# Kernel optimization log

Measured on AMD Instinct MI355X. Metric: run time of the kernel, lower is better.

## Reference

```python
import jax, jax.numpy as jnp
import numpy as np
from jax import lax

K = 5  # up_kernel_size

def nearest_up2(x):
    # PyTorch F.interpolate(scale_factor=2) default mode='nearest': out[i]=in[i//2]
    return jnp.repeat(jnp.repeat(x, 2, axis=2), 2, axis=3)

def conv1x1(x, W, b=None):
    # x: [B,C,H,W], W: [O,C]
    y = jnp.einsum('bchw,oc->bohw', x, W)
    if b is not None:
        y = y + b[None, :, None, None]
    return y

def depthwise3x3(x, W, b):
    # x: [B,25,H,W], W: [25,1,3,3] (OIHW with groups=25)
    y = lax.conv_general_dilated(x, W, window_strides=(1, 1), padding='SAME',
                                 feature_group_count=x.shape[1],
                                 dimension_numbers=('NCHW', 'OIHW', 'NCHW'))
    return y + b[None, :, None, None]

def carafe(de, kernels):
    # de: [B,C,H,W]; kernels: [B,K*K,2H,2W], softmax-normalized over channel dim
    B, C, H, Wd = de.shape
    r = K // 2
    de_p = jnp.pad(de, ((0, 0), (0, 0), (r, r), (r, r)))
    # patches[b,k,c,h,w] = de neighborhood, k = dy*K+dx  -> [B,25,C,H,W]
    patches = jnp.stack([de_p[:, :, dy:dy + H, dx:dx + Wd]
                         for dy in range(K) for dx in range(K)], axis=1)
    # kernels[b,k,2h+s,2w+t] -> [B,25,H,2,W,2]; source pixel is (i//2, j//2)
    kr = kernels.reshape(B, K * K, H, 2, Wd, 2)
    out = jnp.einsum('bkchw,bkhswt->bchswt', patches, kr)
    return out.reshape(B, C, 2 * H, 2 * Wd)

def setup_inputs() -> dict:
    key = jax.random.key(0)
    ks = jax.random.split(key, 8)
    B, C, H, W = 4, 256, 64, 64
    en = jax.random.normal(ks[0], (B, C, 2 * H, 2 * W), dtype=jnp.float32)
    de = jax.random.normal(ks[1], (B, C, H, W), dtype=jnp.float32)
    s = 1.0 / np.sqrt(C)
    W_gate = jax.random.uniform(ks[2], (1, C), jnp.float32, -s, s)
    b_gate = jnp.zeros((1,), jnp.float32)
    W_ce = jax.random.uniform(ks[3], (K * K, C), jnp.float32, -s, s)
    b_ce = jnp.zeros((K * K,), jnp.float32)
    W_cd = jax.random.uniform(ks[4], (K * K, C), jnp.float32, -s, s)
    W_dw = jax.random.uniform(ks[5], (K * K, 1, 3, 3), jnp.float32, -0.33, 0.33)
    b_dw = jnp.zeros((K * K,), jnp.float32)
    return {'en': en, 'de': de, 'W_gate': W_gate, 'b_gate': b_gate,
            'W_ce': W_ce, 'b_ce': b_ce, 'W_cd': W_cd, 'W_dw': W_dw, 'b_dw': b_dw}

def reference(en, de, W_gate, b_gate, W_ce, b_ce, W_cd, W_dw, b_dw):
    # gate generator
    gate = jax.nn.sigmoid(nearest_up2(conv1x1(de, W_gate, b_gate)))  # [B,1,2H,2W]
    # kernel generator (SemiShiftDepthWise)
    enc = conv1x1(en, W_ce, b_ce)      # [B,25,2H,2W]
    dec = conv1x1(de, W_cd)            # [B,25,H,W]
    raw = depthwise3x3(enc, W_dw, b_dw) + nearest_up2(depthwise3x3(dec, W_dw, b_dw))
    kernels = jax.nn.softmax(raw, axis=1)
    return gate * en + (1.0 - gate) * carafe(de, kernels)
```

## Files before the change

kernel.cpp:

```cpp
#include <hip/hip_runtime.h>


typedef unsigned short u16;
typedef unsigned int u32;
typedef float v2f __attribute__((ext_vector_type(2)));

#define NB 4
#define NC 256
#define NH 64
#define NW 64
#define NH2 128
#define NW2 128

#define OFF_WG   0
#define OFF_BG   256
#define OFF_WCE  272
#define OFF_BCE  6672
#define OFF_WCD  6704
#define OFF_WDW  13104
#define OFF_BDW  13330
#define OFF_FLAG 13356

#define OFF_GATE 16384
#define OFF_KB   32768
#define OFF_ENC  851968
#define OFF_DEC  2490368
#define OFF_DET  851968
#define OFF_P1   851968
#define FULL_NEED_BYTES 12877824ull

#define NGATE 16384
#define NDEC  20480
#define NENC  122880
#define NKBF  532480

__device__ __forceinline__ float bf2f(u16 u){ return __uint_as_float(((u32)u) << 16); }
__device__ __forceinline__ u16 f2bf(float f){
  u32 x = __float_as_uint(f);
  return (u16)((x + 0x7fffu + ((x >> 16) & 1u)) >> 16);
}
__device__ __forceinline__ float ldin(const void* p, int i, bool f32){
  return f32 ? ((const float*)p)[i] : bf2f(((const u16*)p)[i]);
}

__global__ __launch_bounds__(256) void k_detect(const void* de_raw, float* ws){
  __shared__ int cnt;
  if (threadIdx.x == 0) cnt = 0;
  __syncthreads();
  int c = 0;
#pragma unroll
  for (int s = 0; s < 2; s++) {
    int i = (threadIdx.x + s * 256) * 2;
    u16 u = ((const u16*)de_raw)[i];
    int e = (u >> 7) & 0xff;
    if (e >= 0x70 && e <= 0x82) c++;
  }
  atomicAdd(&cnt, c);
  __syncthreads();
  if (threadIdx.x == 0) ws[OFF_FLAG] = (cnt < 256) ? 1.0f : 0.0f;
}

__global__ __launch_bounds__(256) void k_prep(const void* Wg, const void* bg,
    const void* Wce, const void* bce, const void* Wcd, const void* Wdw, const void* bdw,
    float* ws){
  bool f = ws[OFF_FLAG] != 0.f;
  int i = threadIdx.x + blockIdx.x * 256;
  if (i < 6400) {
    ws[OFF_WCE + i] = ldin(Wce, i, f);
    ws[OFF_WCD + i] = ldin(Wcd, i, f);
    if (i < 256) ws[OFF_WG + i] = ldin(Wg, i, f);
    if (i < 1)   ws[OFF_BG + i] = ldin(bg, i, f);
    if (i < 25)  ws[OFF_BCE + i] = ldin(bce, i, f);
    if (i < 225) ws[OFF_WDW + i] = ldin(Wdw, i, f);
    if (i < 25)  ws[OFF_BDW + i] = ldin(bdw, i, f);
  }
}


__global__ __launch_bounds__(256) void o1a_dec_gate(const void* de, float* ws){
  __shared__ float red[4][26][64];
  bool f = ws[OFF_FLAG] != 0.f;
  int b = blockIdx.x >> 7;
  int rem = blockIdx.x & 127;
  int h = rem >> 1;
  int chunk = rem & 1;
  int g = threadIdx.x >> 6;
  int w = threadIdx.x & 63;
  int c0 = __builtin_amdgcn_readfirstlane(chunk * 128 + g * 32);
  float acc[26];
#pragma unroll
  for (int o = 0; o < 26; o++) acc[o] = 0.f;
  int idx = ((b * NC + c0) * NH + h) * NW + w;
  for (int ci = 0; ci < 32; ci += 8) {
    float v0 = ldin(de, idx,            f);
    float v1 = ldin(de, idx + 1 * 4096, f);
    float v2 = ldin(de, idx + 2 * 4096, f);
    float v3 = ldin(de, idx + 3 * 4096, f);
    float v4 = ldin(de, idx + 4 * 4096, f);
    float v5 = ldin(de, idx + 5 * 4096, f);
    float v6 = ldin(de, idx + 6 * 4096, f);
    float v7 = ldin(de, idx + 7 * 4096, f);
    idx += 8 * 4096;
    int c = c0 + ci;
    acc[25] += ws[OFF_WG + c] * v0 + ws[OFF_WG + c + 1] * v1
             + ws[OFF_WG + c + 2] * v2 + ws[OFF_WG + c + 3] * v3
             + ws[OFF_WG + c + 4] * v4 + ws[OFF_WG + c + 5] * v5
             + ws[OFF_WG + c + 6] * v6 + ws[OFF_WG + c + 7] * v7;
#pragma unroll
    for (int k = 0; k < 25; k++) {
      const float* wk = ws + OFF_WCD + k * 256 + c;
      acc[k] += wk[0] * v0 + wk[1] * v1 + wk[2] * v2 + wk[3] * v3
              + wk[4] * v4 + wk[5] * v5 + wk[6] * v6 + wk[7] * v7;
    }
  }
#pragma unroll
  for (int o = 0; o < 26; o++) red[g][o][w] = acc[o];
  __syncthreads();
  for (int item = threadIdx.x; item < 26 * 64; item += 256) {
    int o = item >> 6; int ww = item & 63;
    float s = red[0][o][ww] + red[1][o][ww] + red[2][o][ww] + red[3][o][ww];
    ws[OFF_P1 + (((chunk * NB + b) * 26 + o) << 12) + (h << 6) + ww] = s;
  }
}

__global__ __launch_bounds__(256) void o1b_reduce(float* ws){
  int i = blockIdx.x * 256 + threadIdx.x;
  int b = i / (26 * 4096);
  int r = i - b * 26 * 4096;
  int o = r >> 12;
  int pix = r & 4095;
  float s = ws[OFF_P1 + (((0 * NB + b) * 26 + o) << 12) + pix]
          + ws[OFF_P1 + (((1 * NB + b) * 26 + o) << 12) + pix];
  if (o < 25)
    ws[OFF_DEC + ((b * 25 + o) << 12) + pix] = s;
  else {
    float z = s + ws[OFF_BG];
    ws[OFF_GATE + (b << 12) + pix] = 1.f / (1.f + __expf(-z));
  }
}

__global__ __launch_bounds__(256) void o2_det(const void* de, float* ws){
  __shared__ float tile[64][65];
  bool f = ws[OFF_FLAG] != 0.f;
  u16* det = (u16*)(ws + OFF_DET);
  int b = blockIdx.x / 272;
  int r = blockIdx.x % 272;
  int p = r >> 2;
  int c0 = (r & 3) << 6;
  int h = p - 2;
  bool hv = (h >= 0 && h < NH);
  for (int item = threadIdx.x; item < 64 * 64; item += 256) {
    int cl = item >> 6, w = item & 63;
    float v = hv ? ldin(de, ((b * NC + c0 + cl) * NH + h) * NW + w, f) : 0.f;
    tile[w][cl] = v;
  }
  __syncthreads();
  u16* dst = det + ((b * 68 + p) * 68) * NC + c0;
  for (int item = threadIdx.x; item < 68 * 64; item += 256) {
    int q = item >> 6, cl = item & 63;
    int w = q - 2;
    float v = (w >= 0 && w < NW) ? tile[w][cl] : 0.f;
    dst[q * NC + cl] = f2bf(v);
  }
}

__global__ __launch_bounds__(256) void o3_enc(const void* en, float* ws){
  __shared__ float red[4][25][64];
  bool f = ws[OFF_FLAG] != 0.f;
  int b = blockIdx.x >> 8;
  int rem = blockIdx.x & 255;
  int y = rem >> 1;
  int xs = (rem & 1) << 6;
  int g = threadIdx.x >> 6;
  int xl = threadIdx.x & 63;
  int c0 = __builtin_amdgcn_readfirstlane(g * 64);
  float acc[25];
#pragma unroll
  for (int k = 0; k < 25; k++) acc[k] = 0.f;
  int idx = ((b * NC + c0) * NH2 + y) * NW2 + xs + xl;
  for (int ci = 0; ci < 64; ci += 8) {
    float v0 = ldin(en, idx,             f);
    float v1 = ldin(en, idx + 1 * 16384, f);
    float v2 = ldin(en, idx + 2 * 16384, f);
    float v3 = ldin(en, idx + 3 * 16384, f);
    float v4 = ldin(en, idx + 4 * 16384, f);
    float v5 = ldin(en, idx + 5 * 16384, f);
    float v6 = ldin(en, idx + 6 * 16384, f);
    float v7 = ldin(en, idx + 7 * 16384, f);
    idx += 8 * 16384;
    int c = c0 + ci;
#pragma unroll
    for (int k = 0; k < 25; k++) {
      const float* wk = ws + OFF_WCE + k * 256 + c;
      acc[k] += wk[0] * v0 + wk[1] * v1 + wk[2] * v2 + wk[3] * v3
              + wk[4] * v4 + wk[5] * v5 + wk[6] * v6 + wk[7] * v7;
    }
  }
#pragma unroll
  for (int k = 0; k < 25; k++) red[g][k][xl] = acc[k];
  __syncthreads();
  for (int item = threadIdx.x; item < 25 * 64; item += 256) {
    int k = item >> 6; int xx = item & 63;
    float s = red[0][k][xx] + red[1][k][xx] + red[2][k][xx] + red[3][k][xx]
            + ws[OFF_BCE + k];
    ws[OFF_ENC + ((b * 25 + k) * NH2 + y) * NW2 + xs + xx] = s;
  }
}

__global__ __launch_bounds__(256) void o4_kernels(float* ws){
  __shared__ float red[25][64];
  int b = blockIdx.x >> 8;
  int rem = blockIdx.x & 255;
  int y = rem >> 1;
  int xs = (rem & 1) << 6;
  int tg = __builtin_amdgcn_readfirstlane(threadIdx.x >> 6);
  int xl = threadIdx.x & 63;
  int x = xs + xl;
  int h = y >> 1, w = x >> 1;
  const float* enc = ws + OFF_ENC + (b * 25) * NH2 * NW2;
  const float* dec = ws + OFF_DEC + (b * 25) * NH * NW;

  for (int k = tg; k < 25; k += 4) {
    float s = 2.f * ws[OFF_BDW + k];
#pragma unroll
    for (int u = 0; u < 3; u++) {
      int yy = y + u - 1, hh = h + u - 1;
      bool yok = (yy >= 0 && yy < NH2);
      bool hok = (hh >= 0 && hh < NH);
#pragma unroll
      for (int v = 0; v < 3; v++) {
        int xx = x + v - 1, w2 = w + v - 1;
        float wd = ws[OFF_WDW + k * 9 + u * 3 + v];
        if (yok && xx >= 0 && xx < NW2)
          s += enc[(k * NH2 + yy) * NW2 + xx] * wd;
        if (hok && w2 >= 0 && w2 < NW)
          s += dec[(k * NH + hh) * NW + w2] * wd;
      }
    }
    red[k][xl] = s;
  }
  __syncthreads();

  if (threadIdx.x < 64) {
    int t = threadIdx.x;
    int xp = xs + t;
    float m = -1e30f;
#pragma unroll
    for (int k = 0; k < 25; k++) m = fmaxf(m, red[k][t]);
    float sum = 0.f;
#pragma unroll
    for (int k = 0; k < 25; k++) {
      float e = __expf(red[k][t] - m);
      red[k][t] = e;
      sum += e;
    }
    float inv = 1.f / sum;
    int st = ((y & 1) << 1) + (xp & 1);
    int wp = xp >> 1;
    u16* kbu = (u16*)(ws + OFF_KB);
    u16* dst = kbu + ((b * NH + h) * NW + wp) * 100 + st;
#pragma unroll
    for (int k = 0; k < 25; k++) dst[k * 4] = f2bf(red[k][t] * inv);
  }
}

__global__ __launch_bounds__(256) void o5_final(const void* en, float* ws, float* out){
  __shared__ u16 stag[32][260];
  bool f = ws[OFF_FLAG] != 0.f;
  const u16* det = (const u16*)(ws + OFF_DET);
  const u16* kbu = (const u16*)(ws + OFF_KB);
  const float* gate = ws + OFF_GATE;

  int bi = blockIdx.x;
  int xcd = bi & 7;
  int slot = bi >> 3;
  int s = slot & 1;
  int pid = ((slot >> 1) << 3) | xcd;
  int b = pid >> 8;
  int rem = pid & 255;
  int h = rem >> 2;
  int w0b = (rem & 3) * 16;
  int wave = threadIdx.x >> 6;
  int lane = threadIdx.x & 63;
  int c4 = lane * 4;

  int wu0 = __builtin_amdgcn_readfirstlane(w0b + wave * 4);
  const u16* kp0 = kbu + ((b * NH + h) * NW + wu0) * 100 + s * 2;

  v2f acc[4][2][2];
#pragma unroll
  for (int i = 0; i < 4; i++)
#pragma unroll
    for (int t = 0; t < 2; t++)
#pragma unroll
      for (int p = 0; p < 2; p++) { acc[i][t][p].x = 0.f; acc[i][t][p].y = 0.f; }

#pragma unroll
  for (int dy = 0; dy < 5; dy++) {
    const u16* dp = det + (((b * 68 + h + dy) * 68 + wu0) * NC) + c4;
    u32 wlo[8], whi[8];
#pragma unroll
    for (int j = 0; j < 8; j++) {
      uint2 dv = *(const uint2*)(dp + j * NC);
      wlo[j] = dv.x; whi[j] = dv.y;
    }
#pragma unroll
    for (int i = 0; i < 4; i++) {
#pragma unroll
      for (int dx = 0; dx < 5; dx++) {
        int j = i + dx;
        u32 kk = *(const u32*)(kp0 + i * 100 + (dy * 5 + dx) * 4);
        v2f kp2, vA, vB;
        kp2.x = __uint_as_float(kk << 16);
        kp2.y = __uint_as_float(kk & 0xffff0000u);
        vA.x = __uint_as_float(wlo[j] << 16);
        vA.y = __uint_as_float(wlo[j] & 0xffff0000u);
        vB.x = __uint_as_float(whi[j] << 16);
        vB.y = __uint_as_float(whi[j] & 0xffff0000u);
        asm("v_pk_fma_f32 %0, %1, %2, %0 op_sel:[0,0,0] op_sel_hi:[0,1,1]"
            : "+v"(acc[i][0][0]) : "v"(kp2), "v"(vA));
        asm("v_pk_fma_f32 %0, %1, %2, %0 op_sel:[0,0,0] op_sel_hi:[0,1,1]"
            : "+v"(acc[i][0][1]) : "v"(kp2), "v"(vB));
        asm("v_pk_fma_f32 %0, %1, %2, %0 op_sel:[1,0,0] op_sel_hi:[1,1,1]"
            : "+v"(acc[i][1][0]) : "v"(kp2), "v"(vA));
        asm("v_pk_fma_f32 %0, %1, %2, %0 op_sel:[1,0,0] op_sel_hi:[1,1,1]"
            : "+v"(acc[i][1][1]) : "v"(kp2), "v"(vB));
      }
    }
  }

#pragma unroll
  for (int i = 0; i < 4; i++) {
    int xl = (wave * 4 + i) * 2;
#pragma unroll
    for (int t = 0; t < 2; t++) {
      ushort4 pv;
      pv.x = f2bf(acc[i][t][0].x); pv.y = f2bf(acc[i][t][0].y);
      pv.z = f2bf(acc[i][t][1].x); pv.w = f2bf(acc[i][t][1].y);
      *(ushort4*)&stag[xl + t][c4] = pv;
    }
  }
  __syncthreads();

  int xp = threadIdx.x & 31;
  int cb = (threadIdx.x >> 5) * 2;
  int x = w0b * 2 + xp;
  int wpix = w0b + (xp >> 1);
  int y = 2 * h + s;
  float g = gate[(b * NH + h) * NW + wpix];
  float gi = 1.f - g;
#pragma unroll
  for (int pass = 0; pass < 16; pass++) {
    int c = cb + pass * 16;
    u32 rr = *(const u32*)&stag[xp][c];
    float cr0 = bf2f((u16)(rr & 0xffffu));
    float cr1 = bf2f((u16)(rr >> 16));
    int eidx = ((b * NC + c) * NH2 + y) * NW2 + x;
    float e0 = ldin(en, eidx, f);
    float e1 = ldin(en, eidx + NH2 * NW2, f);
    __builtin_nontemporal_store(g * e0 + gi * cr0, &out[eidx]);
    __builtin_nontemporal_store(g * e1 + gi * cr1, &out[eidx + NH2 * NW2]);
  }
}


__global__ __launch_bounds__(256) void kA_gate(const void* de, float* ws, int b){
  bool f = ws[OFF_FLAG] != 0.f;
  int idx = blockIdx.x * 256 + threadIdx.x;
  int h = idx >> 6, w = idx & 63;
  float s = ws[OFF_BG];
  for (int c = 0; c < NC; c++)
    s += ldin(de, ((b * NC + c) * NH + h) * NW + w, f) * ws[OFF_WG + c];
  ws[NGATE + idx] = 1.f / (1.f + __expf(-s));
}

__global__ __launch_bounds__(256) void kB_dec(const void* de, float* ws, int b){
  bool f = ws[OFF_FLAG] != 0.f;
  int idx = blockIdx.x * 256 + threadIdx.x;
  int h = idx >> 6, w = idx & 63;
  float acc[25];
#pragma unroll
  for (int k = 0; k < 25; k++) acc[k] = 0.f;
  for (int c = 0; c < NC; c++) {
    float v = ldin(de, ((b * NC + c) * NH + h) * NW + w, f);
#pragma unroll
    for (int k = 0; k < 25; k++) acc[k] += v * ws[OFF_WCD + k * 256 + c];
  }
#pragma unroll
  for (int k = 0; k < 25; k++)
    ws[NDEC + (k * NH + h) * NW + w] = acc[k];
}

__global__ __launch_bounds__(256) void kC_enc(const void* en, float* ws, int b){
  bool f = ws[OFF_FLAG] != 0.f;
  int idx = blockIdx.x * 256 + threadIdx.x;
  int y = idx >> 7, x = idx & 127;
  float acc[25];
#pragma unroll
  for (int k = 0; k < 25; k++) acc[k] = 0.f;
  for (int c = 0; c < NC; c++) {
    float v = ldin(en, ((b * NC + c) * NH2 + y) * NW2 + x, f);
#pragma unroll
    for (int k = 0; k < 25; k++) acc[k] += v * ws[OFF_WCE + k * 256 + c];
  }
#pragma unroll
  for (int k = 0; k < 25; k++)
    ws[NENC + (k * NH2 + y) * NW2 + x] = acc[k] + ws[OFF_BCE + k];
}

__global__ __launch_bounds__(256) void kD_kern(float* ws){
  int idx = blockIdx.x * 256 + threadIdx.x;
  int y = idx >> 7, x = idx & 127;
  int h = y >> 1, w = x >> 1;
  float raw[25];
#pragma unroll
  for (int k = 0; k < 25; k++) {
    float s = 2.f * ws[OFF_BDW + k];
#pragma unroll
    for (int u = 0; u < 3; u++) {
      int yy = y + u - 1, hh = h + u - 1;
#pragma unroll
      for (int v = 0; v < 3; v++) {
        int xx = x + v - 1, ww = w + v - 1;
        float wd = ws[OFF_WDW + k * 9 + u * 3 + v];
        if (yy >= 0 && yy < NH2 && xx >= 0 && xx < NW2)
          s += ws[NENC + (k * NH2 + yy) * NW2 + xx] * wd;
        if (hh >= 0 && hh < NH && ww >= 0 && ww < NW)
          s += ws[NDEC + (k * NH + hh) * NW + ww] * wd;
      }
    }
    raw[k] = s;
  }
  float m = raw[0];
#pragma unroll
  for (int k = 1; k < 25; k++) m = fmaxf(m, raw[k]);
  float sum = 0.f;
#pragma unroll
  for (int k = 0; k < 25; k++) { raw[k] = __expf(raw[k] - m); sum += raw[k]; }
  float inv = 1.f / sum;
  float* dst = ws + NKBF + idx * 25;
#pragma unroll
  for (int k = 0; k < 25; k++) dst[k] = raw[k] * inv;
}

__global__ __launch_bounds__(256) void kE_out(const void* en, const void* de,
    const float* ws, float* out, int b){
  bool f = ws[OFF_FLAG] != 0.f;
  int idx = blockIdx.x * 256 + threadIdx.x;
  int c = idx >> 14;
  int y = (idx >> 7) & 127;
  int x = idx & 127;
  int h = y >> 1, w = x >> 1;
  const float* kb = ws + NKBF + (y * NW2 + x) * 25;
  float acc = 0.f;
#pragma unroll
  for (int dy = 0; dy < 5; dy++) {
    int hh = h + dy - 2;
    if (hh < 0 || hh >= NH) continue;
#pragma unroll
    for (int dx = 0; dx < 5; dx++) {
      int ww = w + dx - 2;
      if (ww < 0 || ww >= NW) continue;
      acc += ldin(de, ((b * NC + c) * NH + hh) * NW + ww, f) * kb[dy * 5 + dx];
    }
  }
  float g = ws[NGATE + h * NW + w];
  float e = ldin(en, ((b * NC + c) * NH2 + y) * NW2 + x, f);
  out[((b * NC + c) * NH2 + y) * NW2 + x] = g * e + (1.f - g) * acc;
}

static const void* find_by_size(void* const* d_in, const int* in_sizes, int n_in,
                                int want, int skip, const void* fb){
  int seen = 0;
  for (int i = 0; i < n_in; i++)
    if (in_sizes[i] == want) {
      if (seen == skip) return d_in[i];
      seen++;
    }
  return fb;
}

extern "C" void kernel_launch(void* const* d_in, const int* in_sizes, int n_in,
                              void* d_out, int out_size, void* d_ws, size_t ws_size,
                              hipStream_t stream) {
  (void)out_size;
  const void* en  = find_by_size(d_in, in_sizes, n_in, 4*256*128*128, 0, d_in[0]);
  const void* de  = find_by_size(d_in, in_sizes, n_in, 4*256*64*64,   0, d_in[1]);
  const void* Wg  = find_by_size(d_in, in_sizes, n_in, 256,           0, d_in[2]);
  const void* bg  = find_by_size(d_in, in_sizes, n_in, 1,             0, d_in[3]);
  const void* Wce = find_by_size(d_in, in_sizes, n_in, 6400,          0, d_in[4]);
  const void* bce = find_by_size(d_in, in_sizes, n_in, 25,            0, d_in[5]);
  const void* Wcd = find_by_size(d_in, in_sizes, n_in, 6400,          1, d_in[6]);
  const void* Wdw = find_by_size(d_in, in_sizes, n_in, 225,           0, d_in[7]);
  const void* bdw = find_by_size(d_in, in_sizes, n_in, 25,            1, d_in[8]);
  float* ws = (float*)d_ws;
  float* out = (float*)d_out;

  hipLaunchKernelGGL(k_detect, dim3(1), dim3(256), 0, stream, de, ws);
  hipLaunchKernelGGL(k_prep, dim3(25), dim3(256), 0, stream,
                     Wg, bg, Wce, bce, Wcd, Wdw, bdw, ws);

  if (ws_size >= FULL_NEED_BYTES) {
    hipLaunchKernelGGL(o1a_dec_gate, dim3(NB * NH * 2),     dim3(256), 0, stream, de, ws);
    hipLaunchKernelGGL(o1b_reduce,   dim3(1664),            dim3(256), 0, stream, ws);
    hipLaunchKernelGGL(o3_enc,       dim3(NB * NH2 * 2),    dim3(256), 0, stream, en, ws);
    hipLaunchKernelGGL(o4_kernels,   dim3(NB * NH2 * 2),    dim3(256), 0, stream, ws);
    hipLaunchKernelGGL(o2_det,       dim3(NB * 68 * 4),     dim3(256), 0, stream, de, ws);
    hipLaunchKernelGGL(o5_final,     dim3(NB * NH * 4 * 2), dim3(256), 0, stream, en, ws, out);
  } else {
    for (int b = 0; b < NB; b++) {
      hipLaunchKernelGGL(kA_gate, dim3(16),    dim3(256), 0, stream, de, ws, b);
      hipLaunchKernelGGL(kB_dec,  dim3(16),    dim3(256), 0, stream, de, ws, b);
      hipLaunchKernelGGL(kC_enc,  dim3(64),    dim3(256), 0, stream, en, ws, b);
      hipLaunchKernelGGL(kD_kern, dim3(64),    dim3(256), 0, stream, ws);
      hipLaunchKernelGGL(kE_out,  dim3(16384), dim3(256), 0, stream, en, de, ws, out, b);
    }
  }
}
```

Measured before the change: 239.9 us.

## Fuse detect into prep, fold dec reduce into enc, vectorize enc pairs

Merges the dtype-detect kernel into the weight-prep kernel, so each block recomputes the flag locally. Moves the partial-sum reduction for dec/gate into the tail of the enc 1x1 conv kernel, which removes two launches. The enc kernel now processes two adjacent pixels per thread with paired loads and half as many blocks, so each weight load is reused twice. The P1 buffer is moved to a separate workspace region to avoid aliasing ENC, which raises the workspace requirement and the per-thread register pressure.

```diff
diff --git a/kernel.cpp b/kernel.cpp
--- a/kernel.cpp
+++ b/kernel.cpp
@@ -26,8 +26,8 @@
 #define OFF_ENC  851968
 #define OFF_DEC  2490368
 #define OFF_DET  851968
-#define OFF_P1   851968
-#define FULL_NEED_BYTES 12877824ull
+#define OFF_P1   3219456
+#define FULL_NEED_BYTES 16285696ull
 
 #define NGATE 16384
 #define NDEC  20480
@@ -42,8 +42,21 @@
 __device__ __forceinline__ float ldin(const void* p, int i, bool f32){
   return f32 ? ((const float*)p)[i] : bf2f(((const u16*)p)[i]);
 }
-
-__global__ __launch_bounds__(256) void k_detect(const void* de_raw, float* ws){
+__device__ __forceinline__ v2f ldin2(const void* p, int i, bool f32){
+  v2f r;
+  if (f32) {
+    float2 t = *(const float2*)((const float*)p + i);
+    r.x = t.x; r.y = t.y;
+  } else {
+    u32 u = *(const u32*)((const u16*)p + i);
+    r.x = bf2f((u16)(u & 0xffffu)); r.y = bf2f((u16)(u >> 16));
+  }
+  return r;
+}
+
+__global__ __launch_bounds__(256) void k_prep(const void* de_raw,
+    const void* Wg, const void* bg, const void* Wce, const void* bce,
+    const void* Wcd, const void* Wdw, const void* bdw, float* ws){
   __shared__ int cnt;
   if (threadIdx.x == 0) cnt = 0;
   __syncthreads();
@@ -57,13 +70,8 @@
   }
   atomicAdd(&cnt, c);
   __syncthreads();
-  if (threadIdx.x == 0) ws[OFF_FLAG] = (cnt < 256) ? 1.0f : 0.0f;
-}
-
-__global__ __launch_bounds__(256) void k_prep(const void* Wg, const void* bg,
-    const void* Wce, const void* bce, const void* Wcd, const void* Wdw, const void* bdw,
-    float* ws){
-  bool f = ws[OFF_FLAG] != 0.f;
+  bool f = cnt < 256;
+  if (blockIdx.x == 0 && threadIdx.x == 0) ws[OFF_FLAG] = f ? 1.0f : 0.0f;
   int i = threadIdx.x + blockIdx.x * 256;
   if (i < 6400) {
     ws[OFF_WCE + i] = ldin(Wce, i, f);
@@ -123,22 +131,6 @@
   }
 }
 
-__global__ __launch_bounds__(256) void o1b_reduce(float* ws){
-  int i = blockIdx.x * 256 + threadIdx.x;
-  int b = i / (26 * 4096);
-  int r = i - b * 26 * 4096;
-  int o = r >> 12;
-  int pix = r & 4095;
-  float s = ws[OFF_P1 + (((0 * NB + b) * 26 + o) << 12) + pix]
-          + ws[OFF_P1 + (((1 * NB + b) * 26 + o) << 12) + pix];
-  if (o < 25)
-    ws[OFF_DEC + ((b * 25 + o) << 12) + pix] = s;
-  else {
-    float z = s + ws[OFF_BG];
-    ws[OFF_GATE + (b << 12) + pix] = 1.f / (1.f + __expf(-z));
-  }
-}
-
 __global__ __launch_bounds__(256) void o2_det(const void* de, float* ws){
   __shared__ float tile[64][65];
   bool f = ws[OFF_FLAG] != 0.f;
@@ -165,28 +157,26 @@
 }
 
 __global__ __launch_bounds__(256) void o3_enc(const void* en, float* ws){
-  __shared__ float red[4][25][64];
-  bool f = ws[OFF_FLAG] != 0.f;
-  int b = blockIdx.x >> 8;
-  int rem = blockIdx.x & 255;
-  int y = rem >> 1;
-  int xs = (rem & 1) << 6;
+  __shared__ v2f red[4][25][64];
+  bool f = ws[OFF_FLAG] != 0.f;
+  int b = blockIdx.x >> 7;
+  int y = blockIdx.x & 127;
   int g = threadIdx.x >> 6;
   int xl = threadIdx.x & 63;
   int c0 = __builtin_amdgcn_readfirstlane(g * 64);
-  float acc[25];
-#pragma unroll
-  for (int k = 0; k < 25; k++) acc[k] = 0.f;
-  int idx = ((b * NC + c0) * NH2 + y) * NW2 + xs + xl;
+  v2f acc[25];
+#pragma unroll
+  for (int k = 0; k < 25; k++) { acc[k].x = 0.f; acc[k].y = 0.f; }
+  int idx = ((b * NC + c0) * NH2 + y) * NW2 + 2 * xl;
   for (int ci = 0; ci < 64; ci += 8) {
-    float v0 = ldin(en, idx,             f);
-    float v1 = ldin(en, idx + 1 * 16384, f);
-    float v2 = ldin(en, idx + 2 * 16384, f);
-    float v3 = ldin(en, idx + 3 * 16384, f);
-    float v4 = ldin(en, idx + 4 * 16384, f);
-    float v5 = ldin(en, idx + 5 * 16384, f);
-    float v6 = ldin(en, idx + 6 * 16384, f);
-    float v7 = ldin(en, idx + 7 * 16384, f);
+    v2f v0 = ldin2(en, idx,             f);
+    v2f v1 = ldin2(en, idx + 1 * 16384, f);
+    v2f v2 = ldin2(en, idx + 2 * 16384, f);
+    v2f v3 = ldin2(en, idx + 3 * 16384, f);
+    v2f v4 = ldin2(en, idx + 4 * 16384, f);
+    v2f v5 = ldin2(en, idx + 5 * 16384, f);
+    v2f v6 = ldin2(en, idx + 6 * 16384, f);
+    v2f v7 = ldin2(en, idx + 7 * 16384, f);
     idx += 8 * 16384;
     int c = c0 + ci;
 #pragma unroll
@@ -201,9 +191,26 @@
   __syncthreads();
   for (int item = threadIdx.x; item < 25 * 64; item += 256) {
     int k = item >> 6; int xx = item & 63;
-    float s = red[0][k][xx] + red[1][k][xx] + red[2][k][xx] + red[3][k][xx]
-            + ws[OFF_BCE + k];
-    ws[OFF_ENC + ((b * 25 + k) * NH2 + y) * NW2 + xs + xx] = s;
+    v2f s = red[0][k][xx] + red[1][k][xx] + red[2][k][xx] + red[3][k][xx];
+    float bce = ws[OFF_BCE + k];
+    s.x += bce; s.y += bce;
+    *(v2f*)(ws + OFF_ENC + ((b * 25 + k) * NH2 + y) * NW2 + 2 * xx) = s;
+  }
+  int base = blockIdx.x * 832;
+  for (int j = threadIdx.x; j < 832; j += 256) {
+    int i = base + j;
+    int bb = i / (26 * 4096);
+    int r = i - bb * 26 * 4096;
+    int o = r >> 12;
+    int pix = r & 4095;
+    float s = ws[OFF_P1 + (((0 * NB + bb) * 26 + o) << 12) + pix]
+            + ws[OFF_P1 + (((1 * NB + bb) * 26 + o) << 12) + pix];
+    if (o < 25)
+      ws[OFF_DEC + ((bb * 25 + o) << 12) + pix] = s;
+    else {
+      float z = s + ws[OFF_BG];
+      ws[OFF_GATE + (bb << 12) + pix] = 1.f / (1.f + __expf(-z));
+    }
   }
 }
 
@@ -496,14 +503,12 @@
   float* ws = (float*)d_ws;
   float* out = (float*)d_out;
 
-  hipLaunchKernelGGL(k_detect, dim3(1), dim3(256), 0, stream, de, ws);
   hipLaunchKernelGGL(k_prep, dim3(25), dim3(256), 0, stream,
-                     Wg, bg, Wce, bce, Wcd, Wdw, bdw, ws);
+                     de, Wg, bg, Wce, bce, Wcd, Wdw, bdw, ws);
 
   if (ws_size >= FULL_NEED_BYTES) {
     hipLaunchKernelGGL(o1a_dec_gate, dim3(NB * NH * 2),     dim3(256), 0, stream, de, ws);
-    hipLaunchKernelGGL(o1b_reduce,   dim3(1664),            dim3(256), 0, stream, ws);
-    hipLaunchKernelGGL(o3_enc,       dim3(NB * NH2 * 2),    dim3(256), 0, stream, en, ws);
+    hipLaunchKernelGGL(o3_enc,       dim3(NB * NH2),        dim3(256), 0, stream, en, ws);
     hipLaunchKernelGGL(o4_kernels,   dim3(NB * NH2 * 2),    dim3(256), 0, stream, ws);
     hipLaunchKernelGGL(o2_det,       dim3(NB * 68 * 4),     dim3(256), 0, stream, de, ws);
     hipLaunchKernelGGL(o5_final,     dim3(NB * NH * 4 * 2), dim3(256), 0, stream, en, ws, out);
```

Measured after the change: 239.9 us. No clear change (-0.0%).

## Fold detect into prep, merge partial reduce into enc, vectorize final epilogue

Applied to the files above, without the earlier changes.

Removes two kernel launches: the dtype detection now runs inside each prep block, and the decoder/gate partial-sum reduction is appended to the encoder conv kernel, which needs P1 moved to a non-overlapping workspace region and a larger workspace requirement. The final blend now has each thread handle four consecutive x positions, using 16-byte vector loads of en and vector nontemporal stores, with the gate values staged once in shared memory. The aim is less launch overhead and more coalesced, wider memory traffic in the bandwidth-bound last stage. The larger workspace requirement could push execution onto the slow fallback path if the buffer is too small.

```diff
diff --git a/kernel.cpp b/kernel.cpp
--- a/kernel.cpp
+++ b/kernel.cpp
@@ -4,6 +4,7 @@
 typedef unsigned short u16;
 typedef unsigned int u32;
 typedef float v2f __attribute__((ext_vector_type(2)));
+typedef float v4f __attribute__((ext_vector_type(4)));
 
 #define NB 4
 #define NC 256
@@ -26,8 +27,8 @@
 #define OFF_ENC  851968
 #define OFF_DEC  2490368
 #define OFF_DET  851968
-#define OFF_P1   851968
-#define FULL_NEED_BYTES 12877824ull
+#define OFF_P1   3219456
+#define FULL_NEED_BYTES 16285696ull
 
 #define NGATE 16384
 #define NDEC  20480
@@ -42,8 +43,20 @@
 __device__ __forceinline__ float ldin(const void* p, int i, bool f32){
   return f32 ? ((const float*)p)[i] : bf2f(((const u16*)p)[i]);
 }
-
-__global__ __launch_bounds__(256) void k_detect(const void* de_raw, float* ws){
+__device__ __forceinline__ v4f ldin4(const void* p, int i, bool f32){
+  v4f r;
+  if (f32) {
+    r = *(const v4f*)((const float*)p + i);
+  } else {
+    ushort4 u = *(const ushort4*)((const u16*)p + i);
+    r.x = bf2f(u.x); r.y = bf2f(u.y); r.z = bf2f(u.z); r.w = bf2f(u.w);
+  }
+  return r;
+}
+
+__global__ __launch_bounds__(256) void k_prep(const void* de_raw,
+    const void* Wg, const void* bg, const void* Wce, const void* bce,
+    const void* Wcd, const void* Wdw, const void* bdw, float* ws){
   __shared__ int cnt;
   if (threadIdx.x == 0) cnt = 0;
   __syncthreads();
@@ -57,13 +70,8 @@
   }
   atomicAdd(&cnt, c);
   __syncthreads();
-  if (threadIdx.x == 0) ws[OFF_FLAG] = (cnt < 256) ? 1.0f : 0.0f;
-}
-
-__global__ __launch_bounds__(256) void k_prep(const void* Wg, const void* bg,
-    const void* Wce, const void* bce, const void* Wcd, const void* Wdw, const void* bdw,
-    float* ws){
-  bool f = ws[OFF_FLAG] != 0.f;
+  bool f = cnt < 256;
+  if (blockIdx.x == 0 && threadIdx.x == 0) ws[OFF_FLAG] = f ? 1.0f : 0.0f;
   int i = threadIdx.x + blockIdx.x * 256;
   if (i < 6400) {
     ws[OFF_WCE + i] = ldin(Wce, i, f);
@@ -123,22 +131,6 @@
   }
 }
 
-__global__ __launch_bounds__(256) void o1b_reduce(float* ws){
-  int i = blockIdx.x * 256 + threadIdx.x;
-  int b = i / (26 * 4096);
-  int r = i - b * 26 * 4096;
-  int o = r >> 12;
-  int pix = r & 4095;
-  float s = ws[OFF_P1 + (((0 * NB + b) * 26 + o) << 12) + pix]
-          + ws[OFF_P1 + (((1 * NB + b) * 26 + o) << 12) + pix];
-  if (o < 25)
-    ws[OFF_DEC + ((b * 25 + o) << 12) + pix] = s;
-  else {
-    float z = s + ws[OFF_BG];
-    ws[OFF_GATE + (b << 12) + pix] = 1.f / (1.f + __expf(-z));
-  }
-}
-
 __global__ __launch_bounds__(256) void o2_det(const void* de, float* ws){
   __shared__ float tile[64][65];
   bool f = ws[OFF_FLAG] != 0.f;
@@ -205,6 +197,22 @@
             + ws[OFF_BCE + k];
     ws[OFF_ENC + ((b * 25 + k) * NH2 + y) * NW2 + xs + xx] = s;
   }
+  int base = blockIdx.x * 416;
+  for (int j = threadIdx.x; j < 416; j += 256) {
+    int i = base + j;
+    int bb = i / (26 * 4096);
+    int r = i - bb * 26 * 4096;
+    int o = r >> 12;
+    int pix = r & 4095;
+    float s = ws[OFF_P1 + (((0 * NB + bb) * 26 + o) << 12) + pix]
+            + ws[OFF_P1 + (((1 * NB + bb) * 26 + o) << 12) + pix];
+    if (o < 25)
+      ws[OFF_DEC + ((bb * 25 + o) << 12) + pix] = s;
+    else {
+      float z = s + ws[OFF_BG];
+      ws[OFF_GATE + (bb << 12) + pix] = 1.f / (1.f + __expf(-z));
+    }
+  }
 }
 
 __global__ __launch_bounds__(256) void o4_kernels(float* ws){
@@ -266,6 +274,7 @@
 
 __global__ __launch_bounds__(256) void o5_final(const void* en, float* ws, float* out){
   __shared__ u16 stag[32][260];
+  __shared__ float gsh[16];
   bool f = ws[OFF_FLAG] != 0.f;
   const u16* det = (const u16*)(ws + OFF_DET);
   const u16* kbu = (const u16*)(ws + OFF_KB);
@@ -283,6 +292,9 @@
   int wave = threadIdx.x >> 6;
   int lane = threadIdx.x & 63;
   int c4 = lane * 4;
+
+  if (threadIdx.x < 16)
+    gsh[threadIdx.x] = gate[(b * NH + h) * NW + w0b + threadIdx.x];
 
   int wu0 = __builtin_amdgcn_readfirstlane(w0b + wave * 4);
   const u16* kp0 = kbu + ((b * NH + h) * NW + wu0) * 100 + s * 2;
@@ -342,24 +354,28 @@
   }
   __syncthreads();
 
-  int xp = threadIdx.x & 31;
-  int cb = (threadIdx.x >> 5) * 2;
-  int x = w0b * 2 + xp;
-  int wpix = w0b + (xp >> 1);
+  int xq = threadIdx.x & 7;
+  int cc = threadIdx.x >> 3;
+  int x0 = w0b * 2 + xq * 4;
+  int xls = xq * 4;
+  float g0 = gsh[xq * 2], g1 = gsh[xq * 2 + 1];
+  float gi0 = 1.f - g0, gi1 = 1.f - g1;
   int y = 2 * h + s;
-  float g = gate[(b * NH + h) * NW + wpix];
-  float gi = 1.f - g;
-#pragma unroll
-  for (int pass = 0; pass < 16; pass++) {
-    int c = cb + pass * 16;
-    u32 rr = *(const u32*)&stag[xp][c];
-    float cr0 = bf2f((u16)(rr & 0xffffu));
-    float cr1 = bf2f((u16)(rr >> 16));
-    int eidx = ((b * NC + c) * NH2 + y) * NW2 + x;
-    float e0 = ldin(en, eidx, f);
-    float e1 = ldin(en, eidx + NH2 * NW2, f);
-    __builtin_nontemporal_store(g * e0 + gi * cr0, &out[eidx]);
-    __builtin_nontemporal_store(g * e1 + gi * cr1, &out[eidx + NH2 * NW2]);
+#pragma unroll
+  for (int pass = 0; pass < 8; pass++) {
+    int c = cc + pass * 32;
+    float cr0 = bf2f(stag[xls + 0][c]);
+    float cr1 = bf2f(stag[xls + 1][c]);
+    float cr2 = bf2f(stag[xls + 2][c]);
+    float cr3 = bf2f(stag[xls + 3][c]);
+    int eidx = ((b * NC + c) * NH2 + y) * NW2 + x0;
+    v4f e = ldin4(en, eidx, f);
+    v4f o;
+    o.x = g0 * e.x + gi0 * cr0;
+    o.y = g0 * e.y + gi0 * cr1;
+    o.z = g1 * e.z + gi1 * cr2;
+    o.w = g1 * e.w + gi1 * cr3;
+    __builtin_nontemporal_store(o, (v4f*)&out[eidx]);
   }
 }
 
@@ -496,13 +512,11 @@
   float* ws = (float*)d_ws;
   float* out = (float*)d_out;
 
-  hipLaunchKernelGGL(k_detect, dim3(1), dim3(256), 0, stream, de, ws);
   hipLaunchKernelGGL(k_prep, dim3(25), dim3(256), 0, stream,
-                     Wg, bg, Wce, bce, Wcd, Wdw, bdw, ws);
+                     de, Wg, bg, Wce, bce, Wcd, Wdw, bdw, ws);
 
   if (ws_size >= FULL_NEED_BYTES) {
     hipLaunchKernelGGL(o1a_dec_gate, dim3(NB * NH * 2),     dim3(256), 0, stream, de, ws);
-    hipLaunchKernelGGL(o1b_reduce,   dim3(1664),            dim3(256), 0, stream, ws);
     hipLaunchKernelGGL(o3_enc,       dim3(NB * NH2 * 2),    dim3(256), 0, stream, en, ws);
     hipLaunchKernelGGL(o4_kernels,   dim3(NB * NH2 * 2),    dim3(256), 0, stream, ws);
     hipLaunchKernelGGL(o2_det,       dim3(NB * 68 * 4),     dim3(256), 0, stream, de, ws);
```

Result: no change. 238.2 us (-0.7%).
